# Optimization experiments

Hardware: AMD Instinct MI355X
Metric: run time of the kernel (lower is better)

Reference implementation:

```python
import jax, jax.numpy as jnp
import numpy as np
from jax import lax

B, T, N, D = 4, 12, 1024, 128
C_FRONT = 78           # front/back channel split used by the mixup
X_LAST = T // 2 - 1    # static row index of the last (only effective) mixup call
BS_ST = 6              # block_size of mixup_region_ST
SIGMA = 10.0
LN_EPS = 1e-5


def _mixup_region_ST(graph, y):
    """Faithful jax port of mixup_region_ST(graph_front, x=X_LAST, y, 6, sigma=10).
    graph: [T, N, C_FRONT] float; y: traced int scalar."""
    T_, N_, C_ = graph.shape
    x = X_LAST  # static python int
    y_start = jnp.maximum(y - BS_ST, 0)
    y_end = jnp.minimum(y + 2 * BS_ST, N_)

    # temporal gaussian mix of column y over rows [0, x), written at (x, y)
    xs = jnp.arange(x, dtype=graph.dtype)
    w = jnp.exp(-((xs - (x - 1.0)) ** 2) / (2.0 * SIGMA ** 2))
    w = w / w.sum()
    target = graph[:x, y, :]                      # [x, C]
    mixed_value = (w[:, None] * target).sum(0)    # [C]
    g = lax.dynamic_update_slice(graph, mixed_value[None, None, :], (x, y, 0))

    def mix_write(g_, bs, maxj):
        # average blocks g_[:, j*bs:(j+1)*bs, :] for j in [y_start//bs, y_end//bs)
        j0 = y_start // bs
        j1 = y_end // bs
        jj = jnp.arange(maxj)
        mask = (jj < (j1 - j0)).astype(g_.dtype)              # [maxj]
        cols = jnp.clip((j0 + jj)[:, None] * bs + jnp.arange(bs)[None, :], 0, N_ - 1)
        blocks = g_[:, cols, :]                               # [T, maxj, bs, C]
        mixed = (blocks * mask[None, :, None, None]).sum(1) / (j1 - j0).astype(g_.dtype)
        # torch writes mixed_region.to(torch.uint8) into a float tensor
        mixed = lax.stop_gradient(mixed.astype(jnp.uint8).astype(g_.dtype))
        return lax.dynamic_update_slice(g_, mixed, (0, y, 0))

    # torch resets block_size to 1 when y_end > w - block_size
    return lax.cond(y_end > N_ - BS_ST,
                    lambda g_: mix_write(g_, 1, 3 * BS_ST),
                    lambda g_: mix_write(g_, BS_ST, 4),
                    g)


def _forward(inp, adapt_G, xff_w, xff_b, ff1_w, ff1_b, ff2_w, ff2_b, ln_w, ln_b):
    x_ = inp @ xff_w.T + xff_b                       # [B,T,N,3D]
    q, k, v = jnp.split(x_, 3, axis=-1)
    e = jnp.einsum('btnd,btmd->btnm', q, k) / (D ** 0.5)
    e = e @ adapt_G                                  # [B,T,N,N]
    attn = jax.nn.softmax(e, axis=-1)
    attn_det = lax.stop_gradient(attn)               # self.attention_maps = attn.detach()

    def process(attn_b, val_b):                      # [T,N,N], [T,N,D]
        front = val_b[..., :C_FRONT]
        back = val_b[..., C_FRONT:]
        col_sums = attn_b.sum(axis=1)                # [T, N]
        _, idx = lax.top_k(-col_sums, 2)             # 2 smallest per row, ascending
        # only the last loop iteration's mixup survives in the original code
        y = idx[X_LAST, 1]
        return jnp.concatenate([_mixup_region_ST(front, y), back], axis=-1)

    new_value = jax.vmap(process)(attn_det, v)       # [B,T,N,D]
    vi = attn @ new_value                            # [B,T,N,D]
    h = jax.nn.gelu(vi @ ff1_w.T + ff1_b, approximate=False)
    h = h @ ff2_w.T + ff2_b
    out = h + inp
    mu = out.mean(-1, keepdims=True)
    var = ((out - mu) ** 2).mean(-1, keepdims=True)
    return (out - mu) / jnp.sqrt(var + LN_EPS) * ln_w + ln_b


def setup_inputs() -> dict:
    key = jax.random.key(0)
    ks = jax.random.split(key, 6)
    s = 0.02
    return {
        'input': jax.random.normal(ks[0], (B, T, N, D), jnp.float32),
        'adapt_G': jax.random.normal(ks[1], (N, N), jnp.float32) / np.float32(np.sqrt(N)),
        'xff_w': jax.random.normal(ks[2], (3 * D, D), jnp.float32) * s,
        'xff_b': jnp.zeros((3 * D,), jnp.float32),
        'ff1_w': jax.random.normal(ks[3], (D, D), jnp.float32) * s,
        'ff1_b': jnp.zeros((D,), jnp.float32),
        'ff2_w': jax.random.normal(ks[4], (D, D), jnp.float32) * s,
        'ff2_b': jnp.zeros((D,), jnp.float32),
        'ln_w': jnp.ones((D,), jnp.float32),
        'ln_b': jnp.zeros((D,), jnp.float32),
    }


def reference(input, adapt_G, xff_w, xff_b, ff1_w, ff1_b, ff2_w, ff2_b, ln_w, ln_b):
    return _forward(input, adapt_G, xff_w, xff_b, ff1_w, ff1_b, ff2_w, ff2_b, ln_w, ln_b)
```

## Files before the change

### kernel.cpp

```cpp
#include <hip/hip_runtime.h>
#include <hip/hip_bf16.h>

typedef __attribute__((ext_vector_type(8))) short bf16x8;
typedef __attribute__((ext_vector_type(4))) float f32x4;
typedef unsigned long long ull;

#define MFMA(a,b,c) __builtin_amdgcn_mfma_f32_16x16x32_bf16((a),(b),(c),0,0,0)
#define VMCNT(N) asm volatile("s_waitcnt vmcnt(%0)" :: "i"(N) : "memory")

__device__ __forceinline__ short f2bs(float f){
  union { float f; unsigned u; } x; x.f = f;
  unsigned r = (x.u + 0x7fffu + ((x.u >> 16) & 1u)) >> 16;
  return (short)r;
}
__device__ __forceinline__ float bs2f(short s){
  union { unsigned u; float f; } x; x.u = ((unsigned)(unsigned short)s) << 16;
  return x.f;
}

__device__ __forceinline__ void gl2lds16(const void* g, void* l){
  __builtin_amdgcn_global_load_lds((const __attribute__((address_space(1))) void*)g,
                                   (__attribute__((address_space(3))) void*)l, 16, 0, 0);
}

__device__ __forceinline__ void merge2(ull& a1, ull& a2, ull b1, ull b2){
  ull n1 = min(a1, b1);
  ull n2 = min(max(a1, b1), min(a2, b2));
  a1 = n1; a2 = n2;
}

__global__ void conv_kernel(const float* xffw, const float* w1, const float* w2,
                            short* wqkv_b, short* w1_b, short* w2_b){
  int i = blockIdx.x*blockDim.x + threadIdx.x;
  int stride = gridDim.x*blockDim.x;
  for (int idx = i; idx < 384*128; idx += stride) wqkv_b[idx] = f2bs(xffw[idx]);
  for (int idx = i; idx < 128*128; idx += stride) w1_b[idx] = f2bs(w1[idx]);
  for (int idx = i; idx < 128*128; idx += stride) w2_b[idx] = f2bs(w2[idx]);
}

__global__ __launch_bounds__(256) void gtrans_kernel(const float* __restrict__ G,
                                                     short* __restrict__ gt){
  __shared__ float tile[32][33];
  int bx = blockIdx.x & 31;
  int by = blockIdx.x >> 5;
  int tx = threadIdx.x & 31, ty = threadIdx.x >> 5;
  #pragma unroll
  for (int j=0;j<4;j++){
    int n = by*32 + ty + j*8;
    tile[ty+j*8][tx] = G[(size_t)n*1024 + bx*32 + tx];
  }
  __syncthreads();
  #pragma unroll
  for (int j=0;j<4;j++){
    int m = bx*32 + ty + j*8;
    gt[(size_t)m*1024 + by*32 + tx] = f2bs(tile[tx][ty+j*8]);
  }
}

__global__ __launch_bounds__(256,3) void qkv_kernel(const float* __restrict__ inp,
                                                  const short* __restrict__ wqkv,
                                                  const float* __restrict__ bias,
                                                  short* __restrict__ q, short* __restrict__ kT,
                                                  short* __restrict__ nvt){
  __shared__ __align__(16) char smem[49152];
  int w = threadIdx.x >> 6, lane = threadIdx.x & 63;
  int lr = lane & 15, lg = lane >> 4;
  int r0 = blockIdx.x*64;
  int bt = blockIdx.x >> 4;
  int n0 = r0 & 1023;
  int rw = r0 + w*16;
  bf16x8 a[4];
  #pragma unroll
  for (int kc=0;kc<4;kc++){
    const float* ar = inp + (size_t)(rw+lr)*128 + kc*32 + lg*8;
    float4 f0 = *(const float4*)ar;
    float4 f1 = *(const float4*)(ar+4);
    bf16x8 t;
    t[0]=f2bs(f0.x); t[1]=f2bs(f0.y); t[2]=f2bs(f0.z); t[3]=f2bs(f0.w);
    t[4]=f2bs(f1.x); t[5]=f2bs(f1.y); t[6]=f2bs(f1.z); t[7]=f2bs(f1.w);
    a[kc]=t;
  }
  auto stageW = [&](int buf, int kc){
    #pragma unroll
    for (int t=0;t<6;t++){
      int r = (w*6+t)*16 + (lane>>2);
      int s = (lane&3) ^ ((r>>1)&3);
      gl2lds16(wqkv + (size_t)r*128 + kc*32 + s*8,
               smem + buf*24576 + (w*6+t)*1024);
    }
  };
  f32x4 acc[24];
  #pragma unroll
  for (int j=0;j<24;j++) acc[j] = f32x4{0.f,0.f,0.f,0.f};
  stageW(0, 0);
  int cur = 0;
  for (int kc=0; kc<4; kc++){
    if (kc < 3) { stageW(cur^1, kc+1); VMCNT(6); } else { VMCNT(0); }
    __builtin_amdgcn_s_barrier();
    __builtin_amdgcn_sched_barrier(0);
    const char* wb = smem + cur*24576;
    #pragma unroll
    for (int jt=0;jt<24;jt++){
      int j = jt*16 + lr;
      bf16x8 b = *(const bf16x8*)(wb + (size_t)j*64 + ((lg ^ ((lr>>1)&3))*16));
      acc[jt] = MFMA(a[kc], b, acc[jt]);
    }
    __builtin_amdgcn_s_barrier();
    cur ^= 1;
  }
  #pragma unroll
  for (int jt=0;jt<8;jt++){
    float bj = bias[jt*16+lr];
    #pragma unroll
    for (int rr=0;rr<4;rr++)
      q[(size_t)(rw + lg*4 + rr)*128 + jt*16 + lr] = f2bs(acc[jt][rr] + bj);
  }
  __syncthreads();
  short (*tb)[72] = (short(*)[72])smem;
  #pragma unroll
  for (int jt=8;jt<16;jt++){
    int d = (jt-8)*16 + lr;
    float bj = bias[jt*16+lr];
    #pragma unroll
    for (int rr=0;rr<4;rr++) tb[d][w*16 + lg*4 + rr] = f2bs(acc[jt][rr] + bj);
  }
  __syncthreads();
  #pragma unroll
  for (int it=0;it<4;it++){
    int idx = it*256 + threadIdx.x;
    int row = idx >> 3, c8 = (idx & 7)*8;
    *(bf16x8*)(kT + ((size_t)bt*128 + row)*1024 + n0 + c8) = *(const bf16x8*)&tb[row][c8];
  }
  __syncthreads();
  #pragma unroll
  for (int jt=16;jt<24;jt++){
    int c = (jt-16)*16 + lr;
    float bj = bias[jt*16+lr];
    #pragma unroll
    for (int rr=0;rr<4;rr++) tb[c][w*16 + lg*4 + rr] = f2bs(acc[jt][rr] + bj);
  }
  __syncthreads();
  #pragma unroll
  for (int it=0;it<4;it++){
    int idx = it*256 + threadIdx.x;
    int row = idx >> 3, c8 = (idx & 7)*8;
    *(bf16x8*)(nvt + ((size_t)bt*128 + row)*1024 + n0 + c8) = *(const bf16x8*)&tb[row][c8];
  }
}

__global__ __launch_bounds__(256,3) void kg_kernel(const short* __restrict__ gt,
                                                   const short* __restrict__ kT,
                                                   short* __restrict__ kgt){
  __shared__ __align__(16) short gtl[2][64*64];
  __shared__ __align__(16) short ktl[2][128*64];
  int lb = (blockIdx.x & 7)*96 + (blockIdx.x >> 3);
  int bt = lb >> 4;
  int mt = lb & 15;
  int w = threadIdx.x>>6, lane = threadIdx.x&63, lr = lane&15, lg = lane>>4;
  int mblk = mt*64;
  const short* kbase = kT + (size_t)bt*128*1024;
  auto stage = [&](int b, int nc){
    int n0 = nc*64;
    #pragma unroll
    for (int t=0;t<2;t++){
      int row = w*16 + t*8 + (lane>>3);
      int cswz = ((lane&7)*16) ^ ((row&7)<<4);
      gl2lds16(gt + (size_t)(mblk+row)*1024 + n0 + (cswz>>1),
               (char*)gtl[b] + w*2048 + t*1024);
    }
    #pragma unroll
    for (int t=0;t<4;t++){
      int row = w*32 + t*8 + (lane>>3);
      int cswz = ((lane&7)*16) ^ ((row&7)<<4);
      gl2lds16(kbase + (size_t)row*1024 + n0 + (cswz>>1),
               (char*)ktl[b] + w*4096 + t*1024);
    }
  };
  f32x4 acc[8];
  #pragma unroll
  for (int i=0;i<8;i++) acc[i] = f32x4{0.f,0.f,0.f,0.f};
  stage(0, 0);
  int cur = 0;
  for (int nc=0; nc<16; nc++){
    if (nc < 15) { stage(cur^1, nc+1); VMCNT(6); } else { VMCNT(0); }
    __builtin_amdgcn_s_barrier();
    __builtin_amdgcn_sched_barrier(0);
    #pragma unroll
    for (int ks=0;ks<2;ks++){
      int arl = w*16 + lr;
      int acb = ks*64 + lg*16;
      bf16x8 af = *(const bf16x8*)((const char*)gtl[cur] + arl*128 + (acb ^ ((arl&7)<<4)));
      #pragma unroll
      for (int dt=0;dt<8;dt++){
        int brl = dt*16 + lr;
        bf16x8 bf = *(const bf16x8*)((const char*)ktl[cur] + brl*128 + (acb ^ ((brl&7)<<4)));
        acc[dt] = MFMA(af, bf, acc[dt]);
      }
    }
    __builtin_amdgcn_s_barrier();
    cur ^= 1;
  }
  const float SCALE = 0.08838834764831845f;
  int m = mblk + w*16 + lg*4;
  #pragma unroll
  for (int dt=0;dt<8;dt++){
    #pragma unroll
    for (int rr=0;rr<4;rr++){
      kgt[((size_t)(bt*1024 + m + rr))*128 + dt*16 + lr] = f2bs(acc[dt][rr]*SCALE);
    }
  }
}

__global__ __launch_bounds__(256,3) void fused_kernel(const short* __restrict__ q,
                                                      const short* __restrict__ kgt,
                                                      const short* __restrict__ nvt,
                                                      float* __restrict__ zbuf,
                                                      short* __restrict__ pbuf,
                                                      short* __restrict__ vib){
  __shared__ __align__(16) short kgl[64*128];
  __shared__ __align__(16) short nvl[128*64];
  __shared__ __align__(16) short p_lds[4][16][72];
  int lb = (blockIdx.x & 7)*96 + (blockIdx.x >> 3);
  int bt = lb >> 4;
  int rblk = lb & 15;
  int w = threadIdx.x>>6, lane = threadIdx.x&63, lr = lane&15, lg = lane>>4;
  int r0 = rblk*64 + w*16;
  bool is5 = (bt % 12) == 5;
  int bq = bt / 12;
  const short* qrow = q + ((size_t)(bt*1024 + r0 + lr))*128;
  bf16x8 a[4];
  #pragma unroll
  for (int kc=0;kc<4;kc++) a[kc] = *(const bf16x8*)(qrow + kc*32 + lg*8);
  const short* kgb = kgt + (size_t)bt*1024*128;
  const short* nvb = nvt + (size_t)bt*128*1024;
  auto stage_kg = [&](int mc){
    int m0 = mc*64;
    #pragma unroll
    for (int t=0;t<4;t++){
      int row = w*16 + t*4 + (lane>>4);
      int cswz = ((lane&15)*16) ^ ((row&7)<<4);
      gl2lds16(kgb + (size_t)(m0+row)*128 + (cswz>>1),
               (char*)kgl + w*4096 + t*1024);
    }
  };
  auto stage_nv = [&](int mc){
    int m0 = mc*64;
    #pragma unroll
    for (int t=0;t<4;t++){
      int row = w*32 + t*8 + (lane>>3);
      int cswz = ((lane&7)*16) ^ ((row&7)<<4);
      gl2lds16(nvb + (size_t)row*1024 + m0 + (cswz>>1),
               (char*)nvl + w*4096 + t*1024);
    }
  };
  f32x4 acc[8];
  #pragma unroll
  for (int i=0;i<8;i++) acc[i] = f32x4{0.f,0.f,0.f,0.f};
  float zacc[4] = {0.f,0.f,0.f,0.f};
  stage_kg(0);
  stage_nv(0);
  VMCNT(0);
  __builtin_amdgcn_s_barrier();
  __builtin_amdgcn_sched_barrier(0);
  for (int mc=0; mc<16; mc++){
    int m0 = mc*64;
    #pragma unroll
    for (int s=0;s<4;s++){
      f32x4 e = f32x4{0.f,0.f,0.f,0.f};
      #pragma unroll
      for (int kc=0;kc<4;kc++){
        int rl = s*16 + lr;
        int cb = kc*64 + lg*16;
        bf16x8 kb = *(const bf16x8*)((const char*)kgl + rl*256 + (cb ^ ((rl&7)<<4)));
        e = MFMA(a[kc], kb, e);
      }
      #pragma unroll
      for (int rr=0;rr<4;rr++){
        float p = __expf(fminf(e[rr], 60.f));
        zacc[rr] += p;
        p_lds[w][lg*4+rr][s*16+lr] = f2bs(p);
      }
    }
    __builtin_amdgcn_s_barrier();
    if (mc < 15) stage_kg(mc+1);
    if (mc < 15) { VMCNT(4); } else { VMCNT(0); }
    __builtin_amdgcn_s_barrier();
    __builtin_amdgcn_sched_barrier(0);
    bf16x8 pa0 = *(const bf16x8*)&p_lds[w][lr][lg*8];
    bf16x8 pa1 = *(const bf16x8*)&p_lds[w][lr][32+lg*8];
    #pragma unroll
    for (int ct=0; ct<8; ct++){
      int c = ct*16 + lr;
      int mb0 = lg*16;
      int mb1 = 64 + lg*16;
      bf16x8 nb0 = *(const bf16x8*)((const char*)nvl + c*128 + (mb0 ^ ((c&7)<<4)));
      bf16x8 nb1 = *(const bf16x8*)((const char*)nvl + c*128 + (mb1 ^ ((c&7)<<4)));
      acc[ct] = MFMA(pa0, nb0, acc[ct]);
      acc[ct] = MFMA(pa1, nb1, acc[ct]);
    }
    if (is5){
      #pragma unroll
      for (int tt=0; tt<4; tt++){
        int row = tt*4 + (lane>>4);
        int m = (lane&15)*4;
        ull v = *(const ull*)&p_lds[w][row][m];
        *(ull*)(pbuf + ((size_t)bq*1024 + r0 + row)*1024 + m0 + m) = v;
      }
    }
    __builtin_amdgcn_s_barrier();
    if (mc < 15) { stage_nv(mc+1); VMCNT(4); } else { VMCNT(0); }
    __builtin_amdgcn_s_barrier();
    __builtin_amdgcn_sched_barrier(0);
  }
  #pragma unroll
  for (int d=1;d<16;d<<=1){
    #pragma unroll
    for (int rr=0;rr<4;rr++) zacc[rr] += __shfl_xor(zacc[rr], d, 64);
  }
  if (lr==0){
    #pragma unroll
    for (int rr=0;rr<4;rr++) zbuf[(size_t)bt*1024 + r0 + lg*4 + rr] = zacc[rr];
  }
  float inv[4];
  #pragma unroll
  for (int rr=0;rr<4;rr++) inv[rr] = 1.0f/zacc[rr];
  #pragma unroll
  for (int ct=0;ct<8;ct++){
    #pragma unroll
    for (int rr=0;rr<4;rr++){
      vib[((size_t)(bt*1024 + r0 + lg*4 + rr))*128 + ct*16 + lr] = f2bs(acc[ct][rr]*inv[rr]);
    }
  }
}

__global__ __launch_bounds__(256) void colsum_kernel(const short* __restrict__ pbuf,
                                                     const float* __restrict__ zbuf,
                                                     float* __restrict__ csfinal){
  __shared__ float part[4][64];
  int b = blockIdx.x >> 4, mg = blockIdx.x & 15;
  int t = threadIdx.x;
  int mcol = mg*64 + (t & 63);
  int rq = t >> 6;
  const short* pb = pbuf + (size_t)b*1024*1024;
  const float* zb = zbuf + (size_t)(b*12 + 5)*1024;
  float s = 0.f;
  for (int r = rq*256; r < rq*256 + 256; r++){
    s += bs2f(pb[(size_t)r*1024 + mcol]) * (1.0f/zb[r]);
  }
  part[rq][t & 63] = s;
  __syncthreads();
  if (t < 64){
    float cs = (part[0][t] + part[1][t]) + (part[2][t] + part[3][t]);
    csfinal[(size_t)b*1024 + mg*64 + t] = cs;
  }
}

__global__ __launch_bounds__(256) void top2_kernel(const float* __restrict__ csfinal,
                                                   int* __restrict__ yidx){
  __shared__ ull s1[4], s2[4];
  int b = blockIdx.x;
  ull b1 = ~0ull, b2 = ~0ull;
  #pragma unroll
  for (int j=0;j<4;j++){
    int col = j*256 + threadIdx.x;
    float s = csfinal[(size_t)b*1024 + col];
    union { float f; unsigned u; } cv; cv.f = s;
    ull key = ((ull)cv.u << 32) | (unsigned)col;
    merge2(b1, b2, key, ~0ull);
  }
  #pragma unroll
  for (int d=1;d<64;d<<=1){
    ull o1 = __shfl_xor(b1, d, 64);
    ull o2 = __shfl_xor(b2, d, 64);
    merge2(b1, b2, o1, o2);
  }
  int w = threadIdx.x >> 6;
  if ((threadIdx.x & 63) == 0){ s1[w] = b1; s2[w] = b2; }
  __syncthreads();
  if (threadIdx.x == 0){
    ull r1 = s1[0], r2 = s2[0];
    merge2(r1, r2, s1[1], s2[1]);
    merge2(r1, r2, s1[2], s2[2]);
    merge2(r1, r2, s1[3], s2[3]);
    yidx[b] = (int)(r2 & 0xffffffffu);
  }
}

__global__ void nvfixA_kernel(const short* __restrict__ nvt, const int* __restrict__ yidx,
                              float* __restrict__ mixres){
  int bt = blockIdx.x; int b = bt/12, t = bt%12;
  int y = yidx[b];
  int y_start = max(y-6, 0), y_end = min(y+12, 1024);
  int bs, j0, cnt;
  if (y_end > 1024-6){ bs = 1; j0 = y_start; cnt = y_end - y_start; }
  else { bs = 6; j0 = y_start/6; cnt = y_end/6 - j0; }
  int items = bs*78;
  int idx = threadIdx.x;
  if (idx >= items) return;
  int i = idx / 78, c = idx % 78;
  const short* nvb = nvt + (size_t)bt*128*1024;
  float acc = 0.f;
  for (int jj=0;jj<cnt;jj++){
    int col = (j0+jj)*bs + i;
    float gv;
    if (t == 5 && col == y){
      float wsum = 0.f, mv = 0.f;
      #pragma unroll
      for (int tp=0;tp<5;tp++){
        float d = (float)tp - 4.0f;
        float w = __expf(-d*d/200.0f);
        wsum += w;
        mv += w * bs2f(nvt[((size_t)(b*12+tp)*128 + c)*1024 + y]);
      }
      gv = mv / wsum;
    } else {
      gv = bs2f(nvb[(size_t)c*1024 + col]);
    }
    acc += gv;
  }
  mixres[((size_t)bt*6 + i)*78 + c] = acc / (float)cnt;
}

__global__ __launch_bounds__(256) void corr_kernel(const short* __restrict__ q,
                                                   const short* __restrict__ kgt,
                                                   const short* __restrict__ nvt,
                                                   const float* __restrict__ mixres,
                                                   const float* __restrict__ zbuf,
                                                   const int* __restrict__ yidx,
                                                   short* __restrict__ vib){
  __shared__ __align__(16) short kcol[6][128];
  __shared__ float delta[6][78];
  int bt = blockIdx.x >> 2;
  int rc = blockIdx.x & 3;
  int b = bt/12;
  int y = yidx[b];
  int y_end = min(y+12, 1024);
  int bs = (y_end > 1024-6) ? 1 : 6;
  for (int idx = threadIdx.x; idx < 6*128; idx += 256){
    int i = idx >> 7, d = idx & 127;
    kcol[i][d] = (i < bs) ? kgt[((size_t)(bt*1024 + y + i))*128 + d] : (short)0;
  }
  for (int idx = threadIdx.x; idx < 6*78; idx += 256){
    int i = idx / 78, c = idx % 78;
    float dv = 0.f;
    if (i < bs){
      float avg = mixres[((size_t)bt*6 + i)*78 + c];
      int ti = (int)avg;
      unsigned char u = (unsigned char)ti;
      dv = (float)u - bs2f(nvt[((size_t)bt*128 + c)*1024 + (y+i)]);
    }
    delta[i][c] = dv;
  }
  __syncthreads();
  int r = rc*256 + threadIdx.x;
  const short* qr = q + ((size_t)(bt*1024 + r))*128;
  float e[6] = {0.f,0.f,0.f,0.f,0.f,0.f};
  for (int d0 = 0; d0 < 128; d0 += 8){
    bf16x8 qv = *(const bf16x8*)(qr + d0);
    #pragma unroll
    for (int j=0;j<8;j++){
      float qf = bs2f(qv[j]);
      #pragma unroll
      for (int i=0;i<6;i++) e[i] += qf * bs2f(kcol[i][d0+j]);
    }
  }
  float invz = 1.0f / zbuf[(size_t)bt*1024 + r];
  float p[6];
  #pragma unroll
  for (int i=0;i<6;i++) p[i] = (i < bs) ? __expf(fminf(e[i],60.f))*invz : 0.f;
  short* vr = vib + ((size_t)(bt*1024 + r))*128;
  for (int c=0;c<78;c++){
    float dsum = 0.f;
    #pragma unroll
    for (int i=0;i<6;i++) dsum += p[i]*delta[i][c];
    vr[c] = f2bs(bs2f(vr[c]) + dsum);
  }
}

__global__ __launch_bounds__(256,3) void ffn_kernel(const short* __restrict__ vib,
                                                  const float* __restrict__ inp,
                                                  const short* __restrict__ w1b,
                                                  const short* __restrict__ w2b,
                                                  const float* __restrict__ b1,
                                                  const float* __restrict__ b2,
                                                  const float* __restrict__ lnw,
                                                  const float* __restrict__ lnb,
                                                  float* __restrict__ out){
  __shared__ __align__(16) short wl[128*128];
  __shared__ __align__(16) short h_lds[4][16][72];
  int w = threadIdx.x>>6, lane = threadIdx.x&63, lr = lane&15, lg = lane>>4;
  int r0 = blockIdx.x*64 + w*16;
  auto stageW = [&](const short* src){
    #pragma unroll
    for (int t=0;t<8;t++){
      int r = (w*8+t)*4 + (lane>>4);
      int s = (lane&15) ^ (r&7);
      gl2lds16(src + (size_t)r*128 + s*8, (char*)wl + (w*8+t)*1024);
    }
  };
  stageW(w1b);
  bf16x8 a[4];
  #pragma unroll
  for (int kc=0;kc<4;kc++) a[kc] = *(const bf16x8*)(vib + (size_t)(r0+lr)*128 + kc*32 + lg*8);
  __syncthreads();
  f32x4 acc[8];
  #pragma unroll
  for (int i=0;i<8;i++) acc[i] = f32x4{0.f,0.f,0.f,0.f};
  #pragma unroll
  for (int kc=0;kc<4;kc++){
    #pragma unroll
    for (int jt=0;jt<8;jt++){
      bf16x8 b = *(const bf16x8*)((const char*)wl + (size_t)(jt*16+lr)*256 + (((kc*4+lg) ^ (lr&7))*16));
      acc[jt] = MFMA(a[kc], b, acc[jt]);
    }
  }
  #pragma unroll
  for (int jt=0;jt<8;jt++){
    float bj = b1[jt*16+lr];
    #pragma unroll
    for (int rr=0;rr<4;rr++){
      float x = acc[jt][rr] + bj;
      float g = 0.5f*x*(1.0f + erff(x*0.70710678118654752f));
      h_lds[w][lg*4+rr][jt*16+lr] = f2bs(g);
    }
  }
  __syncthreads();
  stageW(w2b);
  bf16x8 ha[4];
  #pragma unroll
  for (int kc=0;kc<4;kc++) ha[kc] = *(const bf16x8*)&h_lds[w][lr][kc*32 + lg*8];
  __syncthreads();
  f32x4 acc2[8];
  #pragma unroll
  for (int i=0;i<8;i++) acc2[i] = f32x4{0.f,0.f,0.f,0.f};
  #pragma unroll
  for (int kc=0;kc<4;kc++){
    #pragma unroll
    for (int jt=0;jt<8;jt++){
      bf16x8 b = *(const bf16x8*)((const char*)wl + (size_t)(jt*16+lr)*256 + (((kc*4+lg) ^ (lr&7))*16));
      acc2[jt] = MFMA(ha[kc], b, acc2[jt]);
    }
  }
  float xv[8][4];
  #pragma unroll
  for (int jt=0;jt<8;jt++){
    float bj = b2[jt*16+lr];
    #pragma unroll
    for (int rr=0;rr<4;rr++){
      xv[jt][rr] = acc2[jt][rr] + bj + inp[(size_t)(r0 + lg*4 + rr)*128 + jt*16 + lr];
    }
  }
  float mu[4], rstd[4];
  #pragma unroll
  for (int rr=0;rr<4;rr++){
    float s = 0.f;
    #pragma unroll
    for (int jt=0;jt<8;jt++) s += xv[jt][rr];
    #pragma unroll
    for (int m=1;m<16;m<<=1) s += __shfl_xor(s, m, 64);
    mu[rr] = s * (1.0f/128.0f);
  }
  #pragma unroll
  for (int rr=0;rr<4;rr++){
    float s = 0.f;
    #pragma unroll
    for (int jt=0;jt<8;jt++){ float d = xv[jt][rr]-mu[rr]; s += d*d; }
    #pragma unroll
    for (int m=1;m<16;m<<=1) s += __shfl_xor(s, m, 64);
    rstd[rr] = rsqrtf(s * (1.0f/128.0f) + 1e-5f);
  }
  #pragma unroll
  for (int jt=0;jt<8;jt++){
    int col = jt*16 + lr;
    float lw = lnw[col], lb = lnb[col];
    #pragma unroll
    for (int rr=0;rr<4;rr++){
      out[(size_t)(r0 + lg*4 + rr)*128 + col] = (xv[jt][rr]-mu[rr])*rstd[rr]*lw + lb;
    }
  }
}

extern "C" void kernel_launch(void* const* d_in, const int* in_sizes, int n_in,
                              void* d_out, int out_size, void* d_ws, size_t ws_size,
                              hipStream_t stream) {
  (void)in_sizes; (void)n_in; (void)out_size;
  const float* inp  = (const float*)d_in[0];
  const float* G    = (const float*)d_in[1];
  const float* xffw = (const float*)d_in[2];
  const float* xffb = (const float*)d_in[3];
  const float* w1   = (const float*)d_in[4];
  const float* b1   = (const float*)d_in[5];
  const float* w2   = (const float*)d_in[6];
  const float* b2   = (const float*)d_in[7];
  const float* lnw  = (const float*)d_in[8];
  const float* lnb  = (const float*)d_in[9];
  float* out = (float*)d_out;
  char* ws = (char*)d_ws;

  size_t off = 0;
  auto take = [&](size_t bytes)->char*{ char* p = ws + off; off += (bytes + 255) & ~(size_t)255; return p; };
  short* wqkv_b = (short*)take(384*128*2);
  short* gt_b   = (short*)take((size_t)1024*1024*2);
  short* w1_b   = (short*)take(128*128*2);
  short* w2_b   = (short*)take(128*128*2);
  short* qb     = (short*)take((size_t)48*1024*128*2);
  short* kTb    = (short*)take((size_t)48*128*1024*2);
  short* nvt    = (short*)take((size_t)48*128*1024*2);
  short* kgt    = (short*)take((size_t)48*1024*128*2);
  float* zbuf   = (float*)take((size_t)48*1024*4);
  short* pbuf   = (short*)take((size_t)4*1024*1024*2);
  float* csfin  = (float*)take((size_t)4*1024*4);
  int*   yidx   = (int*)take(256);
  float* mixres = (float*)take((size_t)48*6*78*4);
  short* vibuf  = (short*)take((size_t)48*1024*128*2);
  if (off > ws_size) return;

  conv_kernel<<<dim3(32), dim3(256), 0, stream>>>(xffw, w1, w2, wqkv_b, w1_b, w2_b);
  gtrans_kernel<<<dim3(1024), dim3(256), 0, stream>>>(G, gt_b);
  qkv_kernel<<<dim3(768), dim3(256), 0, stream>>>(inp, wqkv_b, xffb, qb, kTb, nvt);
  kg_kernel<<<dim3(768), dim3(256), 0, stream>>>(gt_b, kTb, kgt);
  fused_kernel<<<dim3(768), dim3(256), 0, stream>>>(qb, kgt, nvt, zbuf, pbuf, vibuf);
  colsum_kernel<<<dim3(64), dim3(256), 0, stream>>>(pbuf, zbuf, csfin);
  top2_kernel<<<dim3(4), dim3(256), 0, stream>>>(csfin, yidx);
  nvfixA_kernel<<<dim3(48), dim3(512), 0, stream>>>(nvt, yidx, mixres);
  corr_kernel<<<dim3(192), dim3(256), 0, stream>>>(qb, kgt, nvt, mixres, zbuf, yidx, vibuf);
  ffn_kernel<<<dim3(768), dim3(256), 0, stream>>>(vibuf, inp, w1_b, w2_b, b1, b2, lnw, lnb, out);
}
```

Baseline: 157.1 us.

## Merge prep kernels, raise MFMA wave priority, retune fused occupancy and LDS padding

Merges the weight-conversion kernel and the G-transpose kernel into one launch, which removes a kernel launch. Wraps the MFMA inner loops in the qkv, kg, fused and ffn kernels with s_setprio so matrix work gets issue priority over other waves. Raises the fused kernel's launch bound from 3 to 4 blocks and changes the LDS padding of p_lds (removed) and h_lds (widened). Dropping the p_lds padding may add LDS bank conflicts, and the tighter launch bound may cause register spills.

```diff
diff --git a/kernel.cpp b/kernel.cpp
--- a/kernel.cpp
+++ b/kernel.cpp
@@ -29,20 +29,26 @@
   a1 = n1; a2 = n2;
 }
 
-__global__ void conv_kernel(const float* xffw, const float* w1, const float* w2,
-                            short* wqkv_b, short* w1_b, short* w2_b){
-  int i = blockIdx.x*blockDim.x + threadIdx.x;
-  int stride = gridDim.x*blockDim.x;
-  for (int idx = i; idx < 384*128; idx += stride) wqkv_b[idx] = f2bs(xffw[idx]);
-  for (int idx = i; idx < 128*128; idx += stride) w1_b[idx] = f2bs(w1[idx]);
-  for (int idx = i; idx < 128*128; idx += stride) w2_b[idx] = f2bs(w2[idx]);
-}
-
-__global__ __launch_bounds__(256) void gtrans_kernel(const float* __restrict__ G,
-                                                     short* __restrict__ gt){
+__global__ __launch_bounds__(256) void prep_kernel(const float* __restrict__ xffw,
+                                                   const float* __restrict__ w1,
+                                                   const float* __restrict__ w2,
+                                                   const float* __restrict__ G,
+                                                   short* __restrict__ wqkv_b,
+                                                   short* __restrict__ w1_b,
+                                                   short* __restrict__ w2_b,
+                                                   short* __restrict__ gt){
   __shared__ float tile[32][33];
-  int bx = blockIdx.x & 31;
-  int by = blockIdx.x >> 5;
+  int blk = blockIdx.x;
+  if (blk >= 1024){
+    int i = (blk-1024)*256 + threadIdx.x;
+    int stride = 32*256;
+    for (int idx = i; idx < 384*128; idx += stride) wqkv_b[idx] = f2bs(xffw[idx]);
+    for (int idx = i; idx < 128*128; idx += stride) w1_b[idx] = f2bs(w1[idx]);
+    for (int idx = i; idx < 128*128; idx += stride) w2_b[idx] = f2bs(w2[idx]);
+    return;
+  }
+  int bx = blk & 31;
+  int by = blk >> 5;
   int tx = threadIdx.x & 31, ty = threadIdx.x >> 5;
   #pragma unroll
   for (int j=0;j<4;j++){
@@ -99,12 +105,14 @@
     __builtin_amdgcn_s_barrier();
     __builtin_amdgcn_sched_barrier(0);
     const char* wb = smem + cur*24576;
+    __builtin_amdgcn_s_setprio(1);
     #pragma unroll
     for (int jt=0;jt<24;jt++){
       int j = jt*16 + lr;
       bf16x8 b = *(const bf16x8*)(wb + (size_t)j*64 + ((lg ^ ((lr>>1)&3))*16));
       acc[jt] = MFMA(a[kc], b, acc[jt]);
     }
+    __builtin_amdgcn_s_setprio(0);
     __builtin_amdgcn_s_barrier();
     cur ^= 1;
   }
@@ -185,6 +193,7 @@
     if (nc < 15) { stage(cur^1, nc+1); VMCNT(6); } else { VMCNT(0); }
     __builtin_amdgcn_s_barrier();
     __builtin_amdgcn_sched_barrier(0);
+    __builtin_amdgcn_s_setprio(1);
     #pragma unroll
     for (int ks=0;ks<2;ks++){
       int arl = w*16 + lr;
@@ -197,6 +206,7 @@
         acc[dt] = MFMA(af, bf, acc[dt]);
       }
     }
+    __builtin_amdgcn_s_setprio(0);
     __builtin_amdgcn_s_barrier();
     cur ^= 1;
   }
@@ -211,7 +221,7 @@
   }
 }
 
-__global__ __launch_bounds__(256,3) void fused_kernel(const short* __restrict__ q,
+__global__ __launch_bounds__(256,4) void fused_kernel(const short* __restrict__ q,
                                                       const short* __restrict__ kgt,
                                                       const short* __restrict__ nvt,
                                                       float* __restrict__ zbuf,
@@ -219,7 +229,7 @@
                                                       short* __restrict__ vib){
   __shared__ __align__(16) short kgl[64*128];
   __shared__ __align__(16) short nvl[128*64];
-  __shared__ __align__(16) short p_lds[4][16][72];
+  __shared__ __align__(16) short p_lds[4][16][64];
   int lb = (blockIdx.x & 7)*96 + (blockIdx.x >> 3);
   int bt = lb >> 4;
   int rblk = lb & 15;
@@ -264,6 +274,7 @@
   __builtin_amdgcn_sched_barrier(0);
   for (int mc=0; mc<16; mc++){
     int m0 = mc*64;
+    __builtin_amdgcn_s_setprio(1);
     #pragma unroll
     for (int s=0;s<4;s++){
       f32x4 e = f32x4{0.f,0.f,0.f,0.f};
@@ -281,6 +292,7 @@
         p_lds[w][lg*4+rr][s*16+lr] = f2bs(p);
       }
     }
+    __builtin_amdgcn_s_setprio(0);
     __builtin_amdgcn_s_barrier();
     if (mc < 15) stage_kg(mc+1);
     if (mc < 15) { VMCNT(4); } else { VMCNT(0); }
@@ -288,6 +300,7 @@
     __builtin_amdgcn_sched_barrier(0);
     bf16x8 pa0 = *(const bf16x8*)&p_lds[w][lr][lg*8];
     bf16x8 pa1 = *(const bf16x8*)&p_lds[w][lr][32+lg*8];
+    __builtin_amdgcn_s_setprio(1);
     #pragma unroll
     for (int ct=0; ct<8; ct++){
       int c = ct*16 + lr;
@@ -298,6 +311,7 @@
       acc[ct] = MFMA(pa0, nb0, acc[ct]);
       acc[ct] = MFMA(pa1, nb1, acc[ct]);
     }
+    __builtin_amdgcn_s_setprio(0);
     if (is5){
       #pragma unroll
       for (int tt=0; tt<4; tt++){
@@ -487,7 +501,7 @@
                                                   const float* __restrict__ lnb,
                                                   float* __restrict__ out){
   __shared__ __align__(16) short wl[128*128];
-  __shared__ __align__(16) short h_lds[4][16][72];
+  __shared__ __align__(16) short h_lds[4][16][136];
   int w = threadIdx.x>>6, lane = threadIdx.x&63, lr = lane&15, lg = lane>>4;
   int r0 = blockIdx.x*64 + w*16;
   auto stageW = [&](const short* src){
@@ -506,6 +520,7 @@
   f32x4 acc[8];
   #pragma unroll
   for (int i=0;i<8;i++) acc[i] = f32x4{0.f,0.f,0.f,0.f};
+  __builtin_amdgcn_s_setprio(1);
   #pragma unroll
   for (int kc=0;kc<4;kc++){
     #pragma unroll
@@ -514,6 +529,7 @@
       acc[jt] = MFMA(a[kc], b, acc[jt]);
     }
   }
+  __builtin_amdgcn_s_setprio(0);
   #pragma unroll
   for (int jt=0;jt<8;jt++){
     float bj = b1[jt*16+lr];
@@ -533,6 +549,7 @@
   f32x4 acc2[8];
   #pragma unroll
   for (int i=0;i<8;i++) acc2[i] = f32x4{0.f,0.f,0.f,0.f};
+  __builtin_amdgcn_s_setprio(1);
   #pragma unroll
   for (int kc=0;kc<4;kc++){
     #pragma unroll
@@ -541,6 +558,7 @@
       acc2[jt] = MFMA(ha[kc], b, acc2[jt]);
     }
   }
+  __builtin_amdgcn_s_setprio(0);
   float xv[8][4];
   #pragma unroll
   for (int jt=0;jt<8;jt++){
@@ -615,8 +633,7 @@
   short* vibuf  = (short*)take((size_t)48*1024*128*2);
   if (off > ws_size) return;
 
-  conv_kernel<<<dim3(32), dim3(256), 0, stream>>>(xffw, w1, w2, wqkv_b, w1_b, w2_b);
-  gtrans_kernel<<<dim3(1024), dim3(256), 0, stream>>>(G, gt_b);
+  prep_kernel<<<dim3(1056), dim3(256), 0, stream>>>(xffw, w1, w2, G, wqkv_b, w1_b, w2_b, gt_b);
   qkv_kernel<<<dim3(768), dim3(256), 0, stream>>>(inp, wqkv_b, xffb, qb, kTb, nvt);
   kg_kernel<<<dim3(768), dim3(256), 0, stream>>>(gt_b, kTb, kgt);
   fused_kernel<<<dim3(768), dim3(256), 0, stream>>>(qb, kgt, nvt, zbuf, pbuf, vibuf);
```

Result: faster. 153.5 us (-2.3%).
